# Optimization experiments

Measured on AMD Instinct MI355X. Metric: run time of the kernel, lower is better.

The kernel has to match this reference:

```python
import jax, jax.numpy as jnp
import numpy as np
from jax import lax

# Static model/config sizes
B, ANG, C, H, NF, NB = 1, 9, 3, 128, 16, 2


def get_freq_position(n):
    """Anti-diagonal frequency bands of an n x n angular-DCT grid (python/static)."""
    bands = []
    for i in range(n):
        bands.append(([i], [0]))
    for j in range(1, n):
        bands.append(([n - 1], [j]))
    for item in bands:
        while item[0][0] > 0 and item[1][0] < n - 1:
            item[0].insert(0, item[0][0] - 1)
            item[1].insert(0, item[1][0] + 1)
    return bands


def dct_mat(n):
    """Orthonormal DCT-II matrix (row k = k-th basis)."""
    k = jnp.arange(n, dtype=jnp.float32)[:, None]
    i = jnp.arange(n, dtype=jnp.float32)[None, :]
    m = jnp.cos(jnp.pi * (i + 0.5) * k / n) * jnp.sqrt(2.0 / n)
    return m.at[0].multiply(1.0 / np.sqrt(2.0))


def conv3d(x, w, b):
    # x: (N, Cin, D, H, W), w: (Cout, Cin, 3, 3, 3)
    y = lax.conv_general_dilated(x, w, (1, 1, 1), 'SAME',
                                 dimension_numbers=('NCDHW', 'OIDHW', 'NCDHW'))
    return y + b[None, :, None, None, None]


def branch(cut, wi, bi, a, wb, bb):
    """init conv + NB ResBlock3D (PReLU -> Conv3d, residual), plus outer skip."""
    y0 = conv3d(cut, wi, bi)
    y = y0
    for k in range(NB):
        r = jnp.where(y >= 0, y, a[k] * y)  # PReLU (single-parameter)
        y = y + conv3d(r, wb[k], bb[k])
    return y0 + y


def setup_inputs() -> dict:
    key = jax.random.key(0)
    ks = jax.random.split(key, 32)

    def nrm(k, shape, s=0.05):
        return jax.random.normal(k, shape, dtype=jnp.float32) * s

    inp = {"x": jax.random.normal(ks[0], (B, ANG, ANG, C, H, H), dtype=jnp.float32)}
    i = 1
    for n in ("dc", "lo", "mi", "hi"):
        inp[f"w_{n}_i"] = nrm(ks[i], (NF, C, 3, 3, 3)); i += 1
        inp[f"b_{n}_i"] = nrm(ks[i], (NF,)); i += 1
        inp[f"a_{n}"] = jnp.full((NB,), 0.25, dtype=jnp.float32)
        inp[f"w_{n}"] = nrm(ks[i], (NB, NF, NF, 3, 3, 3)); i += 1
        inp[f"b_{n}"] = nrm(ks[i], (NB, NF)); i += 1
    inp["w_last"] = nrm(ks[i], (C, NF))  # 1x1 Conv2d, no bias
    return inp


def reference(x, w_dc_i, b_dc_i, a_dc, w_dc, b_dc,
              w_lo_i, b_lo_i, a_lo, w_lo, b_lo,
              w_mi_i, b_mi_i, a_mi, w_mi, b_mi,
              w_hi_i, b_hi_i, a_hi, w_hi, b_hi, w_last):
    b, u, v, c, h, w = x.shape
    Da = dct_mat(u)  # angular DCT (u == v)
    Ds = dct_mat(h)  # spatial DCT (h == w)

    # SpaAngDCT: spatial 2D DCT then angular 2D DCT
    xf = jnp.einsum('buvchw,Hh,Ww->buvcHW', x, Ds, Ds)
    xf = jnp.einsum('buvchw,Uu,Vv->bUVchw', xf, Da, Da)

    x_rec = jnp.zeros((b, NF, u, v, h, w), dtype=x.dtype)
    for idx, (ui, vi) in enumerate(get_freq_position(u)):
        if idx == 0:
            p = (w_dc_i, b_dc_i, a_dc, w_dc, b_dc)
        elif idx <= 2:
            p = (w_lo_i, b_lo_i, a_lo, w_lo, b_lo)
        elif idx <= u - 1:
            p = (w_mi_i, b_mi_i, a_mi, w_mi, b_mi)
        else:
            p = (w_hi_i, b_hi_i, a_hi, w_hi, b_hi)
        ua, va = jnp.array(ui), jnp.array(vi)
        cut = xf[:, ua, va].transpose(0, 2, 1, 3, 4)  # (b, c, L, h, w)
        out = branch(cut, *p)                          # (b, NF, L, h, w)
        x_rec = x_rec.at[:, :, ua, va].set(out)        # scatter band back

    # 'b c u v h w -> b c (u h) (v w)' then 1x1 conv (NF -> 3)
    xr = x_rec.transpose(0, 1, 2, 4, 3, 5).reshape(b, NF, u * h, v * w)
    xr = jnp.einsum('bnHW,on->boHW', xr, w_last)
    xr = xr.reshape(b, c, u, h, v, w).transpose(0, 2, 4, 1, 3, 5)  # (b,u,v,c,h,w)

    # InverseSpaAngDCT: angular IDCT then spatial IDCT
    xr = jnp.einsum('bUVchw,Uu,Vv->buvchw', xr, Da, Da)
    xr = jnp.einsum('buvcHW,Hh,Ww->buvchw', xr, Ds, Ds)
    return xr + x
```

## Files before the change

kernel.cpp:

```cpp
#include <hip/hip_runtime.h>
#include <hip/hip_bf16.h>
#include <math.h>

typedef __hip_bfloat16 bf16;
typedef __attribute__((ext_vector_type(8))) short short8;
typedef __attribute__((ext_vector_type(4))) float floatx4;
typedef __attribute__((ext_vector_type(4))) unsigned int uint4v;
typedef __attribute__((ext_vector_type(2))) unsigned int uint2v;

#define HW 16384
#define NSLICE 243

__constant__ int c_s_of_p[81] = {
  0, 1,1, 2,2,2, 3,3,3,3, 4,4,4,4,4, 5,5,5,5,5,5, 6,6,6,6,6,6,6,
  7,7,7,7,7,7,7,7, 8,8,8,8,8,8,8,8,8, 9,9,9,9,9,9,9,9,
  10,10,10,10,10,10,10, 11,11,11,11,11,11, 12,12,12,12,12,
  13,13,13,13, 14,14,14, 15,15, 16};
__constant__ int c_l_of_p[81] = {
  0, 0,1, 0,1,2, 0,1,2,3, 0,1,2,3,4, 0,1,2,3,4,5, 0,1,2,3,4,5,6,
  0,1,2,3,4,5,6,7, 0,1,2,3,4,5,6,7,8, 0,1,2,3,4,5,6,7,
  0,1,2,3,4,5,6, 0,1,2,3,4,5, 0,1,2,3,4, 0,1,2,3, 0,1,2, 0,1, 0};
__constant__ int c_L_of_s[17] = {1,2,3,4,5,6,7,8,9,8,7,6,5,4,3,2,1};
__constant__ int c_g_of_s[17] = {0,1,1,2,2,2,2,2,2,3,3,3,3,3,3,3,3};
__constant__ int c_pos_uv[81] = {
  0,1,3,6,10,15,21,28,36,
  2,4,7,11,16,22,29,37,45,
  5,8,12,17,23,30,38,46,53,
  9,13,18,24,31,39,47,54,60,
  14,19,25,32,40,48,55,61,66,
  20,26,33,41,49,56,62,67,71,
  27,34,42,50,57,63,68,72,75,
  35,43,51,58,64,69,73,76,78,
  44,52,59,65,70,74,77,79,80};

struct WPtrs {
  const float* wi[4]; const float* bi[4]; const float* a[4];
  const float* wb[4]; const float* bb[4]; const float* wl;
};

__device__ __forceinline__ unsigned short f2bf(float f) {
  return __bfloat16_as_ushort(__float2bfloat16(f));
}
__device__ __forceinline__ float bflo(unsigned int w) {
  return __uint_as_float(w << 16);
}
__device__ __forceinline__ float bfhi(unsigned int w) {
  return __uint_as_float(w & 0xffff0000u);
}
__device__ __forceinline__ unsigned int pack2(float a, float b) {
  return (unsigned int)f2bf(a) | ((unsigned int)f2bf(b) << 16);
}
__device__ __forceinline__ float invprelu(float v, float invA) {
  return (v >= 0.f) ? v : v * invA;
}
__device__ __forceinline__ void bfsplit(float v, unsigned short& hi, unsigned short& lo) {
  unsigned int bits = __float_as_uint(v);
  hi = (unsigned short)(bits >> 16);
  lo = f2bf(v - __uint_as_float(bits & 0xffff0000u));
}

__global__ __launch_bounds__(256) void k_setup(float* DaF,
                                               unsigned short* TFhi, unsigned short* TFlo,
                                               unsigned short* TIhi, unsigned short* TIlo) {
  const double PI = 3.14159265358979323846;
  int t = blockIdx.x * 256 + threadIdx.x;
  if (t < 81) {
    int U = t / 9, u = t % 9;
    double d = cos(PI * (u + 0.5) * U / 9.0) * sqrt(2.0 / 9.0);
    if (U == 0) d *= (1.0 / sqrt(2.0));
    DaF[t] = (float)d;
  }
  if (t < 16384) {
    int jj = t & 7, lane = (t >> 3) & 63, ks = (t >> 9) & 3, tile = t >> 11;
    int row = tile * 16 + (lane & 15);
    int colk = ks * 32 + (lane >> 4) * 8 + jj;
    double vF = cos(PI * (colk + 0.5) * row / 128.0) * sqrt(2.0 / 128.0);
    if (row == 0) vF *= (1.0 / sqrt(2.0));
    double vI = cos(PI * (row + 0.5) * colk / 128.0) * sqrt(2.0 / 128.0);
    if (colk == 0) vI *= (1.0 / sqrt(2.0));
    unsigned short h, l;
    bfsplit((float)vF, h, l); TFhi[t] = h; TFlo[t] = l;
    bfsplit((float)vI, h, l); TIhi[t] = h; TIlo[t] = l;
  }
}

__global__ __launch_bounds__(256) void k_prep(WPtrs P, unsigned short* Wmf,
                                              float* BiF, float* BbF,
                                              float* AF, float* WlF) {
  int t = blockIdx.x * 256 + threadIdx.x;
  if (t < 92160) {
    int s = t / 7680, r = t % 7680;
    int step = r / 512, r2 = r % 512;
    int lane = r2 >> 3, j = r2 & 7;
    int d = step / 5, i = step % 5;
    int q = lane >> 4, m = lane & 15;
    int tl = 2 * i + (q >> 1);
    int cin = (q & 1) * 8 + j;
    float val = 0.f;
    if (tl <= 8) {
      int ky = tl / 3, kx = tl % 3;
      int tap = d * 9 + ky * 3 + kx;
      if (s < 4) {
        if (cin < 3) val = P.wi[s][(m * 3 + cin) * 27 + tap];
      } else {
        int g = (s - 4) >> 1, k = (s - 4) & 1;
        val = P.wb[g][((k * 16 + m) * 16 + cin) * 27 + tap];
      }
    }
    Wmf[t] = f2bf(val);
  }
  if (t < 64)  BiF[t] = P.bi[t / 16][t % 16];
  if (t < 128) BbF[t] = P.bb[t / 32][t % 32];
  if (t < 8)   AF[t]  = P.a[t / 2][t % 2];
  if (t < 48)  WlF[t] = P.wl[t];
}

__global__ __launch_bounds__(256) void k_dct2(const float* __restrict__ X,
                                              const unsigned short* __restrict__ tabhi,
                                              const unsigned short* __restrict__ tablo,
                                              const float* __restrict__ xres,
                                              float* __restrict__ Y) {
  __shared__ unsigned short sThi[128 * 136];
  __shared__ unsigned short sTlo[128 * 136];
  int s = blockIdx.x;
  int t = threadIdx.x;
  int lane = t & 63, wv = t >> 6;
  int q = lane >> 4, n16 = lane & 15;
  const float* Xs = X + (size_t)s * HW;

  floatx4 acc[2][8];
#pragma unroll
  for (int mt = 0; mt < 2; mt++)
#pragma unroll
    for (int nt = 0; nt < 8; nt++) acc[mt][nt] = (floatx4){0.f, 0.f, 0.f, 0.f};

#pragma unroll
  for (int ks = 0; ks < 4; ks++) {
    short8 ahi[2], alo[2];
#pragma unroll
    for (int mt = 0; mt < 2; mt++) {
      const float* xp = Xs + (wv * 32 + mt * 16 + n16) * 128 + ks * 32 + q * 8;
      float4 a = *(const float4*)xp;
      float4 b = *(const float4*)(xp + 4);
      union { short8 v; unsigned short u[8]; } H, L;
      float xv[8] = {a.x, a.y, a.z, a.w, b.x, b.y, b.z, b.w};
#pragma unroll
      for (int j = 0; j < 8; j++) bfsplit(xv[j], H.u[j], L.u[j]);
      ahi[mt] = H.v; alo[mt] = L.v;
    }
#pragma unroll
    for (int nt = 0; nt < 8; nt++) {
      int e = nt * 2048 + ks * 512 + lane * 8;
      short8 bh = *(const short8*)(tabhi + e);
      short8 bl = *(const short8*)(tablo + e);
#pragma unroll
      for (int mt = 0; mt < 2; mt++) {
        acc[mt][nt] = __builtin_amdgcn_mfma_f32_16x16x32_bf16(ahi[mt], bl, acc[mt][nt], 0, 0, 0);
        acc[mt][nt] = __builtin_amdgcn_mfma_f32_16x16x32_bf16(alo[mt], bh, acc[mt][nt], 0, 0, 0);
        acc[mt][nt] = __builtin_amdgcn_mfma_f32_16x16x32_bf16(ahi[mt], bh, acc[mt][nt], 0, 0, 0);
      }
    }
  }

#pragma unroll
  for (int mt = 0; mt < 2; mt++)
#pragma unroll
    for (int nt = 0; nt < 8; nt++) {
      int col = nt * 16 + n16;
      int rowb = wv * 32 + mt * 16 + q * 4;
#pragma unroll
      for (int rp = 0; rp < 4; rp += 2) {
        unsigned short h0, l0, h1, l1;
        bfsplit(acc[mt][nt][rp], h0, l0);
        bfsplit(acc[mt][nt][rp + 1], h1, l1);
        int widx = (col * 136 + rowb + rp) >> 1;
        ((unsigned int*)sThi)[widx] = (unsigned int)h0 | ((unsigned int)h1 << 16);
        ((unsigned int*)sTlo)[widx] = (unsigned int)l0 | ((unsigned int)l1 << 16);
      }
    }
  __syncthreads();

#pragma unroll
  for (int mt = 0; mt < 2; mt++)
#pragma unroll
    for (int nt = 0; nt < 8; nt++) acc[mt][nt] = (floatx4){0.f, 0.f, 0.f, 0.f};

#pragma unroll
  for (int ks = 0; ks < 4; ks++) {
    short8 ahi[2], alo[2];
#pragma unroll
    for (int mt = 0; mt < 2; mt++) {
      int e = (wv * 2 + mt) * 2048 + ks * 512 + lane * 8;
      ahi[mt] = *(const short8*)(tabhi + e);
      alo[mt] = *(const short8*)(tablo + e);
    }
#pragma unroll
    for (int nt = 0; nt < 8; nt++) {
      int off = (nt * 16 + n16) * 136 + ks * 32 + q * 8;
      short8 bh = *(const short8*)(sThi + off);
      short8 bl = *(const short8*)(sTlo + off);
#pragma unroll
      for (int mt = 0; mt < 2; mt++) {
        acc[mt][nt] = __builtin_amdgcn_mfma_f32_16x16x32_bf16(ahi[mt], bl, acc[mt][nt], 0, 0, 0);
        acc[mt][nt] = __builtin_amdgcn_mfma_f32_16x16x32_bf16(alo[mt], bh, acc[mt][nt], 0, 0, 0);
        acc[mt][nt] = __builtin_amdgcn_mfma_f32_16x16x32_bf16(ahi[mt], bh, acc[mt][nt], 0, 0, 0);
      }
    }
  }

#pragma unroll
  for (int mt = 0; mt < 2; mt++)
#pragma unroll
    for (int nt = 0; nt < 8; nt++) {
      int row0 = wv * 32 + mt * 16 + q * 4;
      int col = nt * 16 + n16;
#pragma unroll
      for (int r = 0; r < 4; r++) {
        size_t oi = (size_t)s * HW + (size_t)(row0 + r) * 128 + col;
        float v = acc[mt][nt][r];
        if (xres) v += xres[oi];
        Y[oi] = v;
      }
    }
}

__global__ __launch_bounds__(256) void k_angu(const float* __restrict__ in,
                                              const float* __restrict__ DaF,
                                              float* __restrict__ out) {
  __shared__ float sDa[81];
  int t = threadIdx.x;
  if (t < 81) sDa[t] = DaF[t];
  __syncthreads();
  int idx = blockIdx.x * 256 + t;
  int hw = idx & (HW - 1);
  int r = idx >> 14;
  int c = r % 3, v = r / 3;
  float f[9];
#pragma unroll
  for (int u = 0; u < 9; u++) f[u] = in[(size_t)((u * 9 + v) * 3 + c) * HW + hw];
#pragma unroll
  for (int U = 0; U < 9; U++) {
    float acc = 0.f;
#pragma unroll
    for (int u = 0; u < 9; u++) acc += sDa[U * 9 + u] * f[u];
    out[(size_t)((U * 9 + v) * 3 + c) * HW + hw] = acc;
  }
}

__global__ __launch_bounds__(256) void k_angv(const float* __restrict__ in,
                                              const float* __restrict__ DaF,
                                              unsigned short* __restrict__ xf2b) {
  __shared__ float sDa[81];
  int t = threadIdx.x;
  if (t < 81) sDa[t] = DaF[t];
  __syncthreads();
  int idx = blockIdx.x * 256 + t;
  int hw = idx & (HW - 1);
  int r = idx >> 14;
  int c = r % 3, U = r / 3;
  float f[9];
#pragma unroll
  for (int v = 0; v < 9; v++) f[v] = in[(size_t)((U * 9 + v) * 3 + c) * HW + hw];
#pragma unroll
  for (int V = 0; V < 9; V++) {
    float acc = 0.f;
#pragma unroll
    for (int v = 0; v < 9; v++) acc += sDa[V * 9 + v] * f[v];
    size_t base = ((size_t)c_pos_uv[U * 9 + V] * HW + hw) * 4;
    xf2b[base + c] = f2bf(acc);
    if (c == 0) xf2b[base + 3] = 0;
  }
}

__global__ __launch_bounds__(256) void k_angvi(const float* __restrict__ xrb,
                                               const float* __restrict__ DaF,
                                               float* __restrict__ out) {
  __shared__ float sDa[81];
  int t = threadIdx.x;
  if (t < 81) sDa[t] = DaF[t];
  __syncthreads();
  int idx = blockIdx.x * 256 + t;
  int hw = idx & (HW - 1);
  int r = idx >> 14;
  int c = r % 3, U = r / 3;
  float f[9];
#pragma unroll
  for (int V = 0; V < 9; V++)
    f[V] = xrb[((size_t)c_pos_uv[U * 9 + V] * 3 + c) * HW + hw];
#pragma unroll
  for (int v = 0; v < 9; v++) {
    float acc = 0.f;
#pragma unroll
    for (int V = 0; V < 9; V++) acc += sDa[V * 9 + v] * f[V];
    out[(size_t)((U * 9 + v) * 3 + c) * HW + hw] = acc;
  }
}

__global__ __launch_bounds__(256) void k_angui(const float* __restrict__ in,
                                               const float* __restrict__ DaF,
                                               float* __restrict__ out) {
  __shared__ float sDa[81];
  int t = threadIdx.x;
  if (t < 81) sDa[t] = DaF[t];
  __syncthreads();
  int idx = blockIdx.x * 256 + t;
  int hw = idx & (HW - 1);
  int r = idx >> 14;
  int c = r % 3, v = r / 3;
  float f[9];
#pragma unroll
  for (int U = 0; U < 9; U++) f[U] = in[(size_t)((U * 9 + v) * 3 + c) * HW + hw];
#pragma unroll
  for (int u = 0; u < 9; u++) {
    float acc = 0.f;
#pragma unroll
    for (int U = 0; U < 9; U++) acc += sDa[U * 9 + u] * f[U];
    out[(size_t)((u * 9 + v) * 3 + c) * HW + hw] = acc;
  }
}

__global__ __launch_bounds__(512) void k_conv(const unsigned short* __restrict__ src,
                                              const unsigned short* __restrict__ prevAct,
                                              const unsigned short* __restrict__ act0,
                                              const unsigned short* __restrict__ Wmf,
                                              const float* __restrict__ BiF,
                                              const float* __restrict__ BbF,
                                              const float* __restrict__ AF,
                                              const float* __restrict__ WlF,
                                              int sel,
                                              unsigned short* __restrict__ boutAct,
                                              float* __restrict__ xrbOut) {
  __shared__ unsigned short s_lds[10 * 132 * 16];
  int p = blockIdx.y;
  int s = c_s_of_p[p], l = c_l_of_p[p];
  int g = c_g_of_s[s], Ls = c_L_of_s[s];
  int row0 = blockIdx.x * 8;
  int t = threadIdx.x;
  int lane = t & 63, wv = t >> 6;
  int q = lane >> 4, n = lane & 15;

  float aNext = (sel < 2) ? AF[g * 2 + sel] : 0.f;
  float invA  = (sel > 0) ? 1.0f / AF[g * 2 + sel - 1] : 0.f;

  int scol = t & 127;
  int shalf = (t >> 7) & 1;
  int srow0 = t >> 8;

  {
    uint4v z = (uint4v){0u, 0u, 0u, 0u};
    int zmax = (sel == 0) ? 1320 : 40;
    for (int i = t; i < zmax; i += 512) {
      int row, half, col;
      if (i < 40) { row = i >> 2; half = (i >> 1) & 1; col = (i & 1) ? 129 : 0; }
      else { int j = i - 40; row = j >> 7; col = (j & 127) + 1; half = 1; }
      *(uint4v*)((char*)s_lds + (size_t)(((row * 2 + half) * 132 + col)) * 16) = z;
    }
  }

  int basel = wv * 4224 + (q & 1) * 2112 + n * 16;
  int off2[5];
#pragma unroll
  for (int i = 0; i < 5; i++) {
    int tl = 2 * i + (q >> 1);
    if (tl > 8) tl = 8;
    int ky = tl / 3, kx = tl % 3;
    off2[i] = basel + ky * 4224 + kx * 16;
  }

  int setIdx = (sel == 0) ? g : (4 + g * 2 + (sel - 1));
  const char* WsetBase = (const char*)Wmf + (size_t)setIdx * 15 * 1024;

  floatx4 acc[8];
#pragma unroll
  for (int cg = 0; cg < 8; cg++) acc[cg] = (floatx4){0.f, 0.f, 0.f, 0.f};

  for (int d = 0; d < 3; d++) {
    int l2 = l + d - 1;
    if (l2 < 0 || l2 >= Ls) continue;
    int p2 = p + d - 1;
    __syncthreads();
    if (sel == 0) {
      if (shalf == 0) {
#pragma unroll
        for (int it = 0; it < 5; it++) {
          int row = srow0 + it * 2;
          int grow = row0 - 1 + row;
          uint2v v2 = (uint2v){0u, 0u};
          if ((unsigned)grow < 128u)
            v2 = *(const uint2v*)(src + ((size_t)p2 * HW + grow * 128 + scol) * 4);
          uint4v val; val.x = v2.x; val.y = v2.y; val.z = 0u; val.w = 0u;
          *(uint4v*)((char*)s_lds + (size_t)((row * 2) * 132 + scol + 1) * 16) = val;
        }
      }
    } else {
#pragma unroll
      for (int it = 0; it < 5; it++) {
        int row = srow0 + it * 2;
        int grow = row0 - 1 + row;
        uint4v val = (uint4v){0u, 0u, 0u, 0u};
        if ((unsigned)grow < 128u)
          val = *(const uint4v*)(src +
              (((size_t)p2 * HW + grow * 128 + scol) * 16 + shalf * 8));
        *(uint4v*)((char*)s_lds + (size_t)((row * 2 + shalf) * 132 + scol + 1) * 16) = val;
      }
    }
    __syncthreads();
    short8 af[5];
#pragma unroll
    for (int i = 0; i < 5; i++)
      af[i] = *(const short8*)(WsetBase + ((d * 5 + i) * 64 + lane) * 16);
#pragma unroll
    for (int cg = 0; cg < 8; cg++) {
#pragma unroll
      for (int i = 0; i < 5; i++) {
        short8 b = *(const short8*)((const char*)s_lds + off2[i] + cg * 256);
        acc[cg] = __builtin_amdgcn_mfma_f32_16x16x32_bf16(af[i], b, acc[cg], 0, 0, 0);
      }
    }
  }

  const float* bp = (sel == 0) ? (BiF + g * 16) : (BbF + g * 32 + (sel - 1) * 16);
  float bz[4];
#pragma unroll
  for (int r = 0; r < 4; r++) bz[r] = bp[q * 4 + r];
  int h = row0 + wv;

  if (sel < 2) {
#pragma unroll
    for (int cg = 0; cg < 8; cg++) {
      size_t pix = (size_t)p * HW + h * 128 + cg * 16 + n;
      float r0 = acc[cg][0] + bz[0], r1 = acc[cg][1] + bz[1];
      float r2 = acc[cg][2] + bz[2], r3 = acc[cg][3] + bz[3];
      if (sel != 0) {
        uint2v pv = *(const uint2v*)(prevAct + pix * 16 + q * 4);
        r0 += invprelu(bflo(pv.x), invA); r1 += invprelu(bfhi(pv.x), invA);
        r2 += invprelu(bflo(pv.y), invA); r3 += invprelu(bfhi(pv.y), invA);
      }
      r0 = fmaxf(r0, 0.f) + aNext * fminf(r0, 0.f);
      r1 = fmaxf(r1, 0.f) + aNext * fminf(r1, 0.f);
      r2 = fmaxf(r2, 0.f) + aNext * fminf(r2, 0.f);
      r3 = fmaxf(r3, 0.f) + aNext * fminf(r3, 0.f);
      uint2v ov; ov.x = pack2(r0, r1); ov.y = pack2(r2, r3);
      *(uint2v*)(boutAct + pix * 16 + q * 4) = ov;
    }
  } else {
    float invA0 = 1.0f / AF[g * 2];
    float wl0[4], wl1[4], wl2[4];
#pragma unroll
    for (int r = 0; r < 4; r++) {
      wl0[r] = WlF[q * 4 + r];
      wl1[r] = WlF[16 + q * 4 + r];
      wl2[r] = WlF[32 + q * 4 + r];
    }
#pragma unroll
    for (int cg = 0; cg < 8; cg++) {
      size_t pix = (size_t)p * HW + h * 128 + cg * 16 + n;
      float r0 = acc[cg][0] + bz[0], r1 = acc[cg][1] + bz[1];
      float r2 = acc[cg][2] + bz[2], r3 = acc[cg][3] + bz[3];
      uint2v pv = *(const uint2v*)(prevAct + pix * 16 + q * 4);
      r0 += invprelu(bflo(pv.x), invA); r1 += invprelu(bfhi(pv.x), invA);
      r2 += invprelu(bflo(pv.y), invA); r3 += invprelu(bfhi(pv.y), invA);
      uint2v p0 = *(const uint2v*)(act0 + pix * 16 + q * 4);
      r0 += invprelu(bflo(p0.x), invA0); r1 += invprelu(bfhi(p0.x), invA0);
      r2 += invprelu(bflo(p0.y), invA0); r3 += invprelu(bfhi(p0.y), invA0);
      float o0 = wl0[0] * r0 + wl0[1] * r1 + wl0[2] * r2 + wl0[3] * r3;
      float o1 = wl1[0] * r0 + wl1[1] * r1 + wl1[2] * r2 + wl1[3] * r3;
      float o2 = wl2[0] * r0 + wl2[1] * r1 + wl2[2] * r2 + wl2[3] * r3;
      o0 += __shfl_xor(o0, 16); o0 += __shfl_xor(o0, 32);
      o1 += __shfl_xor(o1, 16); o1 += __shfl_xor(o1, 32);
      o2 += __shfl_xor(o2, 16); o2 += __shfl_xor(o2, 32);
      if (q == 0) {
        size_t hw = (size_t)h * 128 + cg * 16 + n;
        xrbOut[((size_t)p * 3 + 0) * HW + hw] = o0;
        xrbOut[((size_t)p * 3 + 1) * HW + hw] = o1;
        xrbOut[((size_t)p * 3 + 2) * HW + hw] = o2;
      }
    }
  }
}

extern "C" void kernel_launch(void* const* d_in, const int* in_sizes, int n_in,
                              void* d_out, int out_size, void* d_ws, size_t ws_size,
                              hipStream_t stream) {
  (void)in_sizes; (void)n_in; (void)out_size; (void)ws_size;
  const float* x = (const float*)d_in[0];
  WPtrs P;
  for (int g = 0; g < 4; g++) {
    int b = 1 + g * 5;
    P.wi[g] = (const float*)d_in[b + 0];
    P.bi[g] = (const float*)d_in[b + 1];
    P.a[g]  = (const float*)d_in[b + 2];
    P.wb[g] = (const float*)d_in[b + 3];
    P.bb[g] = (const float*)d_in[b + 4];
  }
  P.wl = (const float*)d_in[21];

  char* base = (char*)d_ws;
  size_t off = 0;
  auto take = [&](size_t bytes) -> char* {
    char* r = base + off;
    off += (bytes + 255) & ~(size_t)255;
    return r;
  };
  float* DaF = (float*)take(81 * 4);
  unsigned short* TFhi = (unsigned short*)take(16384 * 2);
  unsigned short* TFlo = (unsigned short*)take(16384 * 2);
  unsigned short* TIhi = (unsigned short*)take(16384 * 2);
  unsigned short* TIlo = (unsigned short*)take(16384 * 2);
  unsigned short* Wmf = (unsigned short*)take(92160 * 2);
  float* BiF   = (float*)take(256);
  float* BbF   = (float*)take(512);
  float* AF    = (float*)take(32);
  float* WlF   = (float*)take(192);
  float* R1 = (float*)take((size_t)NSLICE * HW * 4);
  float* R2 = (float*)take((size_t)NSLICE * HW * 4);
  float* R3 = (float*)take((size_t)NSLICE * HW * 4);
  unsigned short* braw0 = (unsigned short*)take((size_t)81 * 16 * HW * 2);
  unsigned short* braw1 = (unsigned short*)take((size_t)81 * 16 * HW * 2);
  unsigned short* xf2b = (unsigned short*)R3;
  float* xrb = R3;

  k_setup<<<64, 256, 0, stream>>>(DaF, TFhi, TFlo, TIhi, TIlo);
  k_prep<<<360, 256, 0, stream>>>(P, Wmf, BiF, BbF, AF, WlF);
  k_dct2<<<243, 256, 0, stream>>>(x, TFhi, TFlo, nullptr, R1);
  k_angu<<<1728, 256, 0, stream>>>(R1, DaF, R2);
  k_angv<<<1728, 256, 0, stream>>>(R2, DaF, xf2b);
  k_conv<<<dim3(16, 81), 512, 0, stream>>>(xf2b, nullptr, nullptr, Wmf,
                                           BiF, BbF, AF, WlF, 0, braw0, nullptr);
  k_conv<<<dim3(16, 81), 512, 0, stream>>>(braw0, braw0, nullptr, Wmf,
                                           BiF, BbF, AF, WlF, 1, braw1, nullptr);
  k_conv<<<dim3(16, 81), 512, 0, stream>>>(braw1, braw1, braw0, Wmf,
                                           BiF, BbF, AF, WlF, 2, nullptr, xrb);
  k_angvi<<<1728, 256, 0, stream>>>(xrb, DaF, R2);
  k_angui<<<1728, 256, 0, stream>>>(R2, DaF, R1);
  k_dct2<<<243, 256, 0, stream>>>(R1, TIhi, TIlo, x, (float*)d_out);
}
```

Before: 299.3 us.

## Store angular DCT intermediates in bf16, use global_load_lds in conv, merge setup kernels

The angular DCT and inverse-DCT intermediate buffers are now stored as bf16 instead of fp32, which halves the memory traffic of the angular passes. The conv kernel's main input staging uses direct global-to-LDS loads (global_load_lds) and a padded LDS layout meant to avoid bank conflicts. Out-of-range halo rows are zeroed once up front rather than on every load. The setup and weight-prep kernels are merged into one launch to cut launch overhead. Keeping the intermediates in bf16 costs precision in the forward and inverse angular transforms.

```diff
diff --git a/kernel.cpp b/kernel.cpp
--- a/kernel.cpp
+++ b/kernel.cpp
@@ -41,6 +41,9 @@
 __device__ __forceinline__ unsigned short f2bf(float f) {
   return __bfloat16_as_ushort(__float2bfloat16(f));
 }
+__device__ __forceinline__ float bf2f(unsigned short u) {
+  return __uint_as_float(((unsigned int)u) << 16);
+}
 __device__ __forceinline__ float bflo(unsigned int w) {
   return __uint_as_float(w << 16);
 }
@@ -58,10 +61,21 @@
   hi = (unsigned short)(bits >> 16);
   lo = f2bf(v - __uint_as_float(bits & 0xffff0000u));
 }
-
-__global__ __launch_bounds__(256) void k_setup(float* DaF,
-                                               unsigned short* TFhi, unsigned short* TFlo,
-                                               unsigned short* TIhi, unsigned short* TIlo) {
+__device__ __forceinline__ void gl_lds16(const void* g, void* l) {
+  __builtin_amdgcn_global_load_lds(
+      (const __attribute__((address_space(1))) unsigned int*)g,
+      (__attribute__((address_space(3))) unsigned int*)l, 16, 0, 0);
+}
+__device__ __forceinline__ int ldsoff(int plane, int col) {
+  return plane * 2112 + ((plane & 3) << 5) + (col << 4);
+}
+
+__global__ __launch_bounds__(256) void k_init(WPtrs P, float* DaF,
+                                              unsigned short* TFhi, unsigned short* TFlo,
+                                              unsigned short* TIhi, unsigned short* TIlo,
+                                              unsigned short* Wmf,
+                                              float* BiF, float* BbF,
+                                              float* AF, float* WlF) {
   const double PI = 3.14159265358979323846;
   int t = blockIdx.x * 256 + threadIdx.x;
   if (t < 81) {
@@ -82,12 +96,6 @@
     bfsplit((float)vF, h, l); TFhi[t] = h; TFlo[t] = l;
     bfsplit((float)vI, h, l); TIhi[t] = h; TIlo[t] = l;
   }
-}
-
-__global__ __launch_bounds__(256) void k_prep(WPtrs P, unsigned short* Wmf,
-                                              float* BiF, float* BbF,
-                                              float* AF, float* WlF) {
-  int t = blockIdx.x * 256 + threadIdx.x;
   if (t < 92160) {
     int s = t / 7680, r = t % 7680;
     int step = r / 512, r2 = r % 512;
@@ -119,7 +127,8 @@
                                               const unsigned short* __restrict__ tabhi,
                                               const unsigned short* __restrict__ tablo,
                                               const float* __restrict__ xres,
-                                              float* __restrict__ Y) {
+                                              float* __restrict__ Yf,
+                                              unsigned short* __restrict__ Ybf) {
   __shared__ unsigned short sThi[128 * 136];
   __shared__ unsigned short sTlo[128 * 136];
   int s = blockIdx.x;
@@ -218,15 +227,19 @@
       for (int r = 0; r < 4; r++) {
         size_t oi = (size_t)s * HW + (size_t)(row0 + r) * 128 + col;
         float v = acc[mt][nt][r];
-        if (xres) v += xres[oi];
-        Y[oi] = v;
-      }
-    }
-}
-
-__global__ __launch_bounds__(256) void k_angu(const float* __restrict__ in,
+        if (Ybf) {
+          Ybf[oi] = f2bf(v);
+        } else {
+          if (xres) v += xres[oi];
+          Yf[oi] = v;
+        }
+      }
+    }
+}
+
+__global__ __launch_bounds__(256) void k_angu(const unsigned short* __restrict__ in,
                                               const float* __restrict__ DaF,
-                                              float* __restrict__ out) {
+                                              unsigned short* __restrict__ out) {
   __shared__ float sDa[81];
   int t = threadIdx.x;
   if (t < 81) sDa[t] = DaF[t];
@@ -237,17 +250,17 @@
   int c = r % 3, v = r / 3;
   float f[9];
 #pragma unroll
-  for (int u = 0; u < 9; u++) f[u] = in[(size_t)((u * 9 + v) * 3 + c) * HW + hw];
+  for (int u = 0; u < 9; u++) f[u] = bf2f(in[(size_t)((u * 9 + v) * 3 + c) * HW + hw]);
 #pragma unroll
   for (int U = 0; U < 9; U++) {
     float acc = 0.f;
 #pragma unroll
     for (int u = 0; u < 9; u++) acc += sDa[U * 9 + u] * f[u];
-    out[(size_t)((U * 9 + v) * 3 + c) * HW + hw] = acc;
-  }
-}
-
-__global__ __launch_bounds__(256) void k_angv(const float* __restrict__ in,
+    out[(size_t)((U * 9 + v) * 3 + c) * HW + hw] = f2bf(acc);
+  }
+}
+
+__global__ __launch_bounds__(256) void k_angv(const unsigned short* __restrict__ in,
                                               const float* __restrict__ DaF,
                                               unsigned short* __restrict__ xf2b) {
   __shared__ float sDa[81];
@@ -260,7 +273,7 @@
   int c = r % 3, U = r / 3;
   float f[9];
 #pragma unroll
-  for (int v = 0; v < 9; v++) f[v] = in[(size_t)((U * 9 + v) * 3 + c) * HW + hw];
+  for (int v = 0; v < 9; v++) f[v] = bf2f(in[(size_t)((U * 9 + v) * 3 + c) * HW + hw]);
 #pragma unroll
   for (int V = 0; V < 9; V++) {
     float acc = 0.f;
@@ -274,7 +287,7 @@
 
 __global__ __launch_bounds__(256) void k_angvi(const float* __restrict__ xrb,
                                                const float* __restrict__ DaF,
-                                               float* __restrict__ out) {
+                                               unsigned short* __restrict__ out) {
   __shared__ float sDa[81];
   int t = threadIdx.x;
   if (t < 81) sDa[t] = DaF[t];
@@ -292,11 +305,11 @@
     float acc = 0.f;
 #pragma unroll
     for (int V = 0; V < 9; V++) acc += sDa[V * 9 + v] * f[V];
-    out[(size_t)((U * 9 + v) * 3 + c) * HW + hw] = acc;
-  }
-}
-
-__global__ __launch_bounds__(256) void k_angui(const float* __restrict__ in,
+    out[(size_t)((U * 9 + v) * 3 + c) * HW + hw] = f2bf(acc);
+  }
+}
+
+__global__ __launch_bounds__(256) void k_angui(const unsigned short* __restrict__ in,
                                                const float* __restrict__ DaF,
                                                float* __restrict__ out) {
   __shared__ float sDa[81];
@@ -309,7 +322,7 @@
   int c = r % 3, v = r / 3;
   float f[9];
 #pragma unroll
-  for (int U = 0; U < 9; U++) f[U] = in[(size_t)((U * 9 + v) * 3 + c) * HW + hw];
+  for (int U = 0; U < 9; U++) f[U] = bf2f(in[(size_t)((U * 9 + v) * 3 + c) * HW + hw]);
 #pragma unroll
   for (int u = 0; u < 9; u++) {
     float acc = 0.f;
@@ -330,7 +343,7 @@
                                               int sel,
                                               unsigned short* __restrict__ boutAct,
                                               float* __restrict__ xrbOut) {
-  __shared__ unsigned short s_lds[10 * 132 * 16];
+  __shared__ unsigned short s_lds[21184];
   int p = blockIdx.y;
   int s = c_s_of_p[p], l = c_l_of_p[p];
   int g = c_g_of_s[s], Ls = c_L_of_s[s];
@@ -353,18 +366,26 @@
       int row, half, col;
       if (i < 40) { row = i >> 2; half = (i >> 1) & 1; col = (i & 1) ? 129 : 0; }
       else { int j = i - 40; row = j >> 7; col = (j & 127) + 1; half = 1; }
-      *(uint4v*)((char*)s_lds + (size_t)(((row * 2 + half) * 132 + col)) * 16) = z;
-    }
-  }
-
-  int basel = wv * 4224 + (q & 1) * 2112 + n * 16;
+      *(uint4v*)((char*)s_lds + ldsoff(row * 2 + half, col)) = z;
+    }
+    for (int row = 0; row < 10; row++) {
+      int grow = row0 - 1 + row;
+      if ((unsigned)grow >= 128u) {
+        for (int i = t; i < 264; i += 512) {
+          int half = i / 132, col = i % 132;
+          *(uint4v*)((char*)s_lds + ldsoff(row * 2 + half, col)) = z;
+        }
+      }
+    }
+  }
+
   int off2[5];
 #pragma unroll
   for (int i = 0; i < 5; i++) {
     int tl = 2 * i + (q >> 1);
     if (tl > 8) tl = 8;
     int ky = tl / 3, kx = tl % 3;
-    off2[i] = basel + ky * 4224 + kx * 16;
+    off2[i] = ldsoff(2 * (wv + ky) + (q & 1), n + kx);
   }
 
   int setIdx = (sel == 0) ? g : (4 + g * 2 + (sel - 1));
@@ -385,11 +406,11 @@
         for (int it = 0; it < 5; it++) {
           int row = srow0 + it * 2;
           int grow = row0 - 1 + row;
-          uint2v v2 = (uint2v){0u, 0u};
-          if ((unsigned)grow < 128u)
-            v2 = *(const uint2v*)(src + ((size_t)p2 * HW + grow * 128 + scol) * 4);
-          uint4v val; val.x = v2.x; val.y = v2.y; val.z = 0u; val.w = 0u;
-          *(uint4v*)((char*)s_lds + (size_t)((row * 2) * 132 + scol + 1) * 16) = val;
+          if ((unsigned)grow < 128u) {
+            uint2v v2 = *(const uint2v*)(src + ((size_t)p2 * HW + grow * 128 + scol) * 4);
+            uint4v val; val.x = v2.x; val.y = v2.y; val.z = 0u; val.w = 0u;
+            *(uint4v*)((char*)s_lds + ldsoff(row * 2, scol + 1)) = val;
+          }
         }
       }
     } else {
@@ -397,11 +418,13 @@
       for (int it = 0; it < 5; it++) {
         int row = srow0 + it * 2;
         int grow = row0 - 1 + row;
-        uint4v val = (uint4v){0u, 0u, 0u, 0u};
-        if ((unsigned)grow < 128u)
-          val = *(const uint4v*)(src +
-              (((size_t)p2 * HW + grow * 128 + scol) * 16 + shalf * 8));
-        *(uint4v*)((char*)s_lds + (size_t)((row * 2 + shalf) * 132 + scol + 1) * 16) = val;
+        if ((unsigned)grow < 128u) {
+          const void* gp = (const void*)(src +
+              (((size_t)p2 * HW + (size_t)grow * 128 + scol) * 16 + shalf * 8));
+          void* lp = (void*)((char*)s_lds +
+              ldsoff(row * 2 + shalf, (wv & 1) * 64 + 1));
+          gl_lds16(gp, lp);
+        }
       }
     }
     __syncthreads();
@@ -513,25 +536,26 @@
   float* AF    = (float*)take(32);
   float* WlF   = (float*)take(192);
   float* R1 = (float*)take((size_t)NSLICE * HW * 4);
-  float* R2 = (float*)take((size_t)NSLICE * HW * 4);
+  unsigned short* B1 = (unsigned short*)take((size_t)NSLICE * HW * 2);
+  unsigned short* B2 = (unsigned short*)take((size_t)NSLICE * HW * 2);
   float* R3 = (float*)take((size_t)NSLICE * HW * 4);
   unsigned short* braw0 = (unsigned short*)take((size_t)81 * 16 * HW * 2);
   unsigned short* braw1 = (unsigned short*)take((size_t)81 * 16 * HW * 2);
   unsigned short* xf2b = (unsigned short*)R3;
   float* xrb = R3;
 
-  k_setup<<<64, 256, 0, stream>>>(DaF, TFhi, TFlo, TIhi, TIlo);
-  k_prep<<<360, 256, 0, stream>>>(P, Wmf, BiF, BbF, AF, WlF);
-  k_dct2<<<243, 256, 0, stream>>>(x, TFhi, TFlo, nullptr, R1);
-  k_angu<<<1728, 256, 0, stream>>>(R1, DaF, R2);
-  k_angv<<<1728, 256, 0, stream>>>(R2, DaF, xf2b);
+  k_init<<<360, 256, 0, stream>>>(P, DaF, TFhi, TFlo, TIhi, TIlo,
+                                  Wmf, BiF, BbF, AF, WlF);
+  k_dct2<<<243, 256, 0, stream>>>(x, TFhi, TFlo, nullptr, nullptr, B1);
+  k_angu<<<1728, 256, 0, stream>>>(B1, DaF, B2);
+  k_angv<<<1728, 256, 0, stream>>>(B2, DaF, xf2b);
   k_conv<<<dim3(16, 81), 512, 0, stream>>>(xf2b, nullptr, nullptr, Wmf,
                                            BiF, BbF, AF, WlF, 0, braw0, nullptr);
   k_conv<<<dim3(16, 81), 512, 0, stream>>>(braw0, braw0, nullptr, Wmf,
                                            BiF, BbF, AF, WlF, 1, braw1, nullptr);
   k_conv<<<dim3(16, 81), 512, 0, stream>>>(braw1, braw1, braw0, Wmf,
                                            BiF, BbF, AF, WlF, 2, nullptr, xrb);
-  k_angvi<<<1728, 256, 0, stream>>>(xrb, DaF, R2);
-  k_angui<<<1728, 256, 0, stream>>>(R2, DaF, R1);
-  k_dct2<<<243, 256, 0, stream>>>(R1, TIhi, TIlo, x, (float*)d_out);
-}
+  k_angvi<<<1728, 256, 0, stream>>>(xrb, DaF, B1);
+  k_angui<<<1728, 256, 0, stream>>>(B1, DaF, R1);
+  k_dct2<<<243, 256, 0, stream>>>(R1, TIhi, TIlo, x, (float*)d_out, nullptr);
+}
```

Result: faster. 290.3 us (-3.0%).
